# Optimization experiments

Hardware: AMD Instinct MI355X
Metric: run time of the kernel (lower is better)

The kernel has to match this reference:

```python
import jax, jax.numpy as jnp
import numpy as np

B, F, V, D, A, ND = 4096, 26, 100000, 16, 16, 13


def setup_inputs() -> dict:
    key = jax.random.key(0)
    ks = jax.random.split(key, 10)
    dense_input = jax.random.normal(ks[0], (B, ND), dtype=jnp.float32)
    sparse_input = jax.random.randint(ks[1], (B, F), 0, V, dtype=jnp.int32)
    # all fields share feat_num=V, so stack tables into one [F, V, D] array
    embed_tables = jax.random.normal(ks[2], (F, V, D), dtype=jnp.float32) * 0.001
    att_W = jax.random.normal(ks[3], (D, A), dtype=jnp.float32) * (2.0 / (D + A)) ** 0.5
    att_b = jnp.zeros((A,), dtype=jnp.float32)
    att_h = jax.random.normal(ks[4], (A, 1), dtype=jnp.float32) * (2.0 / (A + 1)) ** 0.5
    att_p = jax.random.normal(ks[5], (D, 1), dtype=jnp.float32) * (2.0 / (D + 1)) ** 0.5
    lin_w_dense = jax.random.normal(ks[6], (ND, 1), dtype=jnp.float32) * 0.01
    lin_w_sparse = jax.random.normal(ks[7], (F * D, 1), dtype=jnp.float32) * 0.01
    lin_b = jnp.zeros((1,), dtype=jnp.float32)
    return {"dense_input": dense_input, "sparse_input": sparse_input,
            "embed_tables": embed_tables, "att_W": att_W, "att_b": att_b,
            "att_h": att_h, "att_p": att_p, "lin_w_dense": lin_w_dense,
            "lin_w_sparse": lin_w_sparse, "lin_b": lin_b}


def reference(dense_input, sparse_input, embed_tables, att_W, att_b, att_h,
              att_p, lin_w_dense, lin_w_sparse, lin_b):
    # per-field embedding gather: [B, F, D]
    emb = embed_tables[jnp.arange(F)[None, :], sparse_input]
    sparse_concat = emb.reshape(B, F * D)
    # linear part (Linear(dense, sparse_concat) -> [B, 1])
    linear_result = dense_input @ lin_w_dense + sparse_concat @ lin_w_sparse + lin_b
    # pairwise element-wise products for i < j: [B, P, D], P = F*(F-1)/2
    iu, ju = np.triu_indices(F, k=1)
    ewp = emb[:, iu, :] * emb[:, ju, :]
    # attention MLP over pairs
    att_wx_b = jax.nn.relu(jnp.einsum('bpd,da->bpa', ewp, att_W) + att_b)
    score = jax.nn.softmax(jnp.einsum('bpa,ao->bpo', att_wx_b, att_h), axis=1)  # [B,P,1]
    att_output = jnp.sum(score * ewp, axis=1)  # [B, D]; dropout_rate=0 -> identity
    afm_result = att_output @ att_p  # [B, 1]
    return jax.nn.sigmoid(afm_result + linear_result)
```

## Files before the change

kernel.cpp:

```cpp
#include <hip/hip_runtime.h>
#include <hip/hip_bf16.h>

typedef float v4f    __attribute__((ext_vector_type(4)));
typedef float f32x16 __attribute__((ext_vector_type(16)));
typedef __bf16 bf16x8 __attribute__((ext_vector_type(8)));

#define BATCH 4096
#define NF 26
#define NV 100000
#define ND_ 16
#define NA 16
#define NDENSE 13
#define NPAIR 325
#define ROWP 20
#define WPB 4
#define BLOCK (WPB * 64)
#define NTILE 11

__global__ __launch_bounds__(BLOCK) void afm_kernel(
    const float* __restrict__ dense,
    const int*   __restrict__ sparse,
    const float* __restrict__ tables,
    const float* __restrict__ attW,
    const float* __restrict__ attB,
    const float* __restrict__ attH,
    const float* __restrict__ attP,
    const float* __restrict__ wDense,
    const float* __restrict__ wSparse,
    const float* __restrict__ linB,
    float* __restrict__ out)
{
    __shared__ int sOFF[NPAIR];
    __shared__ __align__(16) float sEmb[WPB][NF * ROWP];
    __shared__ int sIdx[WPB][NF];

    const int tid  = threadIdx.x;
    const int wave = tid >> 6;
    const int lane = tid & 63;
    const int col  = lane & 31;
    const int hi   = lane >> 5;
    const int b    = blockIdx.x * WPB + wave;

    for (int p = tid; p < NPAIR; p += BLOCK) {
        int i = 0, rem = p;
        while (rem >= NF - 1 - i) { rem -= NF - 1 - i; ++i; }
        const int j = i + 1 + rem;
        sOFF[p] = (i * ROWP) | ((j * ROWP) << 16);
    }
    if (lane < NF) sIdx[wave][lane] = sparse[b * NF + lane];
    __syncthreads();

    for (int c = lane; c < (NF * ND_) / 4; c += 64) {
        const int f  = c >> 2;
        const int d4 = (c & 3) << 2;
        const float4 v = *reinterpret_cast<const float4*>(
            tables + ((size_t)f * NV + (size_t)sIdx[wave][f]) * ND_ + d4);
        *reinterpret_cast<float4*>(&sEmb[wave][f * ROWP + d4]) = v;
    }

    bf16x8 afrag;
    #pragma unroll
    for (int t = 0; t < 8; ++t) {
        float a = 0.f;
        if (col < NA)       a = attW[(hi * 8 + t) * NA + col];
        else if (col == NA) a = attP[hi * 8 + t];
        afrag[t] = (__bf16)a;
    }
    float  hreg[8];
    f32x16 cinit = {0.f,0.f,0.f,0.f,0.f,0.f,0.f,0.f,0.f,0.f,0.f,0.f,0.f,0.f,0.f,0.f};
    #pragma unroll
    for (int r = 0; r < 8; ++r) {
        const int k = (r & 3) + 8 * (r >> 2) + 4 * hi;
        hreg[r]  = attH[k];
        cinit[r] = attB[k];
    }

    const float* __restrict__ semb = sEmb[wave];

    float lin = 0.f;
    for (int e = lane; e < NF * ND_; e += 64)
        lin += semb[(e >> 4) * ROWP + (e & 15)] * wSparse[e];
    if (lane < NDENSE)
        lin += dense[b * NDENSE + lane] * wDense[lane];

    float num = 0.f, den = 0.f;
    for (int t = 0; t < NTILE; ++t) {
        const int p     = t * 32 + col;
        const bool valid = (p < NPAIR) && (hi == 0);
        const int pc    = (p < NPAIR) ? p : (NPAIR - 1);
        const int offs  = sOFF[pc];
        const float* ri = semb + (offs & 0xffff) + hi * 8;
        const float* rj = semb + (offs >> 16)    + hi * 8;

        const v4f x0 = *reinterpret_cast<const v4f*>(ri);
        const v4f x1 = *reinterpret_cast<const v4f*>(ri + 4);
        const v4f y0 = *reinterpret_cast<const v4f*>(rj);
        const v4f y1 = *reinterpret_cast<const v4f*>(rj + 4);
        const v4f e0 = x0 * y0;
        const v4f e1 = x1 * y1;

        bf16x8 bfrag;
        bfrag[0] = (__bf16)e0[0]; bfrag[1] = (__bf16)e0[1];
        bfrag[2] = (__bf16)e0[2]; bfrag[3] = (__bf16)e0[3];
        bfrag[4] = (__bf16)e1[0]; bfrag[5] = (__bf16)e1[1];
        bfrag[6] = (__bf16)e1[2]; bfrag[7] = (__bf16)e1[3];

        const f32x16 acc =
            __builtin_amdgcn_mfma_f32_32x32x16_bf16(afrag, bfrag, cinit, 0, 0, 0);

        float sp = 0.f;
        #pragma unroll
        for (int r = 0; r < 8; ++r)
            sp = fmaf(fmaxf(acc[r], 0.f), hreg[r], sp);
        const float sfull = sp + __shfl_xor(sp, 32);

        const float ev = valid ? __expf(sfull) : 0.f;
        num = fmaf(ev, acc[8], num);
        den += ev;
    }

    #pragma unroll
    for (int o = 32; o; o >>= 1) {
        num += __shfl_xor(num, o);
        den += __shfl_xor(den, o);
        lin += __shfl_xor(lin, o);
    }
    if (lane == 0) {
        const float x = num / den + lin + linB[0];
        out[b] = 1.f / (1.f + __expf(-x));
    }
}

extern "C" void kernel_launch(void* const* d_in, const int* in_sizes, int n_in,
                              void* d_out, int out_size, void* d_ws, size_t ws_size,
                              hipStream_t stream) {
    const float* dense   = (const float*)d_in[0];
    const int*   sparse  = (const int*)d_in[1];
    const float* tables  = (const float*)d_in[2];
    const float* attW    = (const float*)d_in[3];
    const float* attB    = (const float*)d_in[4];
    const float* attH    = (const float*)d_in[5];
    const float* attP    = (const float*)d_in[6];
    const float* wDense  = (const float*)d_in[7];
    const float* wSparse = (const float*)d_in[8];
    const float* linB    = (const float*)d_in[9];
    float* out = (float*)d_out;

    const int grid = BATCH / WPB;
    afm_kernel<<<grid, BLOCK, 0, stream>>>(
        dense, sparse, tables, attW, attB, attH, attP,
        wDense, wSparse, linB, out);
}
```

Measured before the change: 15.41 us.

## Drop block barrier and pair table; walk contiguous pairs per lane with cached row

Removes the shared pair-offset table and the block-wide __syncthreads. Sparse indices now stay in registers and reach the gather lanes through a wave shuffle, with only a wave barrier before reading the embeddings. Each lane now handles a contiguous run of pairs, stepping (i, j) incrementally and reloading row i only when it changes, which cuts LDS reads and removes the division-like pair decode from every tile. The trade-off is more divergence when lanes cross row boundaries at different tiles, and reliance on the wave barrier being enough to make the LDS writes visible within the wave.

New measurement: 28.71 us. +86.3%, slower.

```diff
diff --git a/kernel.cpp b/kernel.cpp
--- a/kernel.cpp
+++ b/kernel.cpp
@@ -30,9 +30,7 @@
     const float* __restrict__ linB,
     float* __restrict__ out)
 {
-    __shared__ int sOFF[NPAIR];
     __shared__ __align__(16) float sEmb[WPB][NF * ROWP];
-    __shared__ int sIdx[WPB][NF];
 
     const int tid  = threadIdx.x;
     const int wave = tid >> 6;
@@ -41,21 +39,20 @@
     const int hi   = lane >> 5;
     const int b    = blockIdx.x * WPB + wave;
 
-    for (int p = tid; p < NPAIR; p += BLOCK) {
-        int i = 0, rem = p;
-        while (rem >= NF - 1 - i) { rem -= NF - 1 - i; ++i; }
-        const int j = i + 1 + rem;
-        sOFF[p] = (i * ROWP) | ((j * ROWP) << 16);
-    }
-    if (lane < NF) sIdx[wave][lane] = sparse[b * NF + lane];
-    __syncthreads();
+    int idxreg = 0;
+    if (lane < NF) idxreg = sparse[b * NF + lane];
 
-    for (int c = lane; c < (NF * ND_) / 4; c += 64) {
-        const int f  = c >> 2;
-        const int d4 = (c & 3) << 2;
-        const float4 v = *reinterpret_cast<const float4*>(
-            tables + ((size_t)f * NV + (size_t)sIdx[wave][f]) * ND_ + d4);
-        *reinterpret_cast<float4*>(&sEmb[wave][f * ROWP + d4]) = v;
+    #pragma unroll
+    for (int rnd = 0; rnd < 2; ++rnd) {
+        const int c = lane + rnd * 64;
+        if (c < (NF * ND_) / 4) {
+            const int f  = c >> 2;
+            const int d4 = (c & 3) << 2;
+            const int row = __shfl(idxreg, f);
+            const float4 v = *reinterpret_cast<const float4*>(
+                tables + ((size_t)f * NV + (size_t)row) * ND_ + d4);
+            *reinterpret_cast<float4*>(&sEmb[wave][f * ROWP + d4]) = v;
+        }
     }
 
     bf16x8 afrag;
@@ -75,29 +72,42 @@
         cinit[r] = attB[k];
     }
 
+    __builtin_amdgcn_wave_barrier();
+
     const float* __restrict__ semb = sEmb[wave];
 
     float lin = 0.f;
-    for (int e = lane; e < NF * ND_; e += 64)
-        lin += semb[(e >> 4) * ROWP + (e & 15)] * wSparse[e];
+    #pragma unroll
+    for (int rnd = 0; rnd < 7; ++rnd) {
+        const int e = lane + rnd * 64;
+        if (e < NF * ND_)
+            lin += semb[(e >> 4) * ROWP + (e & 15)] * wSparse[e];
+    }
     if (lane < NDENSE)
         lin += dense[b * NDENSE + lane] * wDense[lane];
 
+    int p0 = col * NTILE;
+    if (p0 > NPAIR - 1) p0 = NPAIR - 1;
+    int i = 0, rem = p0;
+    while (rem >= NF - 1 - i) { rem -= NF - 1 - i; ++i; }
+    int j = i + 1 + rem;
+
     float num = 0.f, den = 0.f;
+    v4f ri0, ri1;
+    bool need_ri = true;
+
     for (int t = 0; t < NTILE; ++t) {
-        const int p     = t * 32 + col;
-        const bool valid = (p < NPAIR) && (hi == 0);
-        const int pc    = (p < NPAIR) ? p : (NPAIR - 1);
-        const int offs  = sOFF[pc];
-        const float* ri = semb + (offs & 0xffff) + hi * 8;
-        const float* rj = semb + (offs >> 16)    + hi * 8;
-
-        const v4f x0 = *reinterpret_cast<const v4f*>(ri);
-        const v4f x1 = *reinterpret_cast<const v4f*>(ri + 4);
+        if (need_ri) {
+            const float* ri = semb + i * ROWP + hi * 8;
+            ri0 = *reinterpret_cast<const v4f*>(ri);
+            ri1 = *reinterpret_cast<const v4f*>(ri + 4);
+            need_ri = false;
+        }
+        const float* rj = semb + j * ROWP + hi * 8;
         const v4f y0 = *reinterpret_cast<const v4f*>(rj);
         const v4f y1 = *reinterpret_cast<const v4f*>(rj + 4);
-        const v4f e0 = x0 * y0;
-        const v4f e1 = x1 * y1;
+        const v4f e0 = ri0 * y0;
+        const v4f e1 = ri1 * y1;
 
         bf16x8 bfrag;
         bfrag[0] = (__bf16)e0[0]; bfrag[1] = (__bf16)e0[1];
@@ -114,9 +124,17 @@
             sp = fmaf(fmaxf(acc[r], 0.f), hreg[r], sp);
         const float sfull = sp + __shfl_xor(sp, 32);
 
+        const bool valid = (col * NTILE + t < NPAIR) && (hi == 0);
         const float ev = valid ? __expf(sfull) : 0.f;
         num = fmaf(ev, acc[8], num);
         den += ev;
+
+        ++j;
+        if (j >= NF) {
+            if (i < NF - 2) { ++i; }
+            j = i + 1;
+            need_ri = true;
+        }
     }
 
     #pragma unroll
```

## Issue embedding gathers before setup and broadcast indices via shuffles

Applied to the files above, without the earlier changes.

Each wave keeps its sparse indices in registers and broadcasts them with wave shuffles instead of staging them in shared memory. That lets the embedding gathers start at kernel entry, before the pair-offset table and weight fragments are built, and the block barrier moves after that setup so gather latency overlaps it. The linear-term loop and the MFMA tile loop are fully unrolled. The ReLU·h reduction is written as packed 2-wide FMAs to encourage packed FP32 instructions. Unrolling raises register pressure and code size.

Result: faster. 14.87 us (-3.5%).

```diff
diff --git a/kernel.cpp b/kernel.cpp
--- a/kernel.cpp
+++ b/kernel.cpp
@@ -1,6 +1,7 @@
 #include <hip/hip_runtime.h>
 #include <hip/hip_bf16.h>
 
+typedef float v2f    __attribute__((ext_vector_type(2)));
 typedef float v4f    __attribute__((ext_vector_type(4)));
 typedef float f32x16 __attribute__((ext_vector_type(16)));
 typedef __bf16 bf16x8 __attribute__((ext_vector_type(8)));
@@ -32,7 +33,6 @@
 {
     __shared__ int sOFF[NPAIR];
     __shared__ __align__(16) float sEmb[WPB][NF * ROWP];
-    __shared__ int sIdx[WPB][NF];
 
     const int tid  = threadIdx.x;
     const int wave = tid >> 6;
@@ -41,21 +41,27 @@
     const int hi   = lane >> 5;
     const int b    = blockIdx.x * WPB + wave;
 
+    int idxreg = 0;
+    if (lane < NF) idxreg = sparse[b * NF + lane];
+
+    #pragma unroll
+    for (int rnd = 0; rnd < 2; ++rnd) {
+        const int c = lane + rnd * 64;
+        if (c < (NF * ND_) / 4) {
+            const int f  = c >> 2;
+            const int d4 = (c & 3) << 2;
+            const int row = __shfl(idxreg, f);
+            const float4 v = *reinterpret_cast<const float4*>(
+                tables + ((size_t)f * NV + (size_t)row) * ND_ + d4);
+            *reinterpret_cast<float4*>(&sEmb[wave][f * ROWP + d4]) = v;
+        }
+    }
+
     for (int p = tid; p < NPAIR; p += BLOCK) {
         int i = 0, rem = p;
         while (rem >= NF - 1 - i) { rem -= NF - 1 - i; ++i; }
         const int j = i + 1 + rem;
         sOFF[p] = (i * ROWP) | ((j * ROWP) << 16);
-    }
-    if (lane < NF) sIdx[wave][lane] = sparse[b * NF + lane];
-    __syncthreads();
-
-    for (int c = lane; c < (NF * ND_) / 4; c += 64) {
-        const int f  = c >> 2;
-        const int d4 = (c & 3) << 2;
-        const float4 v = *reinterpret_cast<const float4*>(
-            tables + ((size_t)f * NV + (size_t)sIdx[wave][f]) * ND_ + d4);
-        *reinterpret_cast<float4*>(&sEmb[wave][f * ROWP + d4]) = v;
     }
 
     bf16x8 afrag;
@@ -75,15 +81,22 @@
         cinit[r] = attB[k];
     }
 
+    __syncthreads();
+
     const float* __restrict__ semb = sEmb[wave];
 
     float lin = 0.f;
-    for (int e = lane; e < NF * ND_; e += 64)
-        lin += semb[(e >> 4) * ROWP + (e & 15)] * wSparse[e];
+    #pragma unroll
+    for (int rnd = 0; rnd < 7; ++rnd) {
+        const int e = lane + rnd * 64;
+        if (e < NF * ND_)
+            lin += semb[(e >> 4) * ROWP + (e & 15)] * wSparse[e];
+    }
     if (lane < NDENSE)
         lin += dense[b * NDENSE + lane] * wDense[lane];
 
     float num = 0.f, den = 0.f;
+    #pragma unroll
     for (int t = 0; t < NTILE; ++t) {
         const int p     = t * 32 + col;
         const bool valid = (p < NPAIR) && (hi == 0);
@@ -108,10 +121,15 @@
         const f32x16 acc =
             __builtin_amdgcn_mfma_f32_32x32x16_bf16(afrag, bfrag, cinit, 0, 0, 0);
 
-        float sp = 0.f;
+        v2f sp2 = {0.f, 0.f};
         #pragma unroll
-        for (int r = 0; r < 8; ++r)
-            sp = fmaf(fmaxf(acc[r], 0.f), hreg[r], sp);
+        for (int r = 0; r < 4; ++r) {
+            v2f z;  z.x = acc[2 * r];  z.y = acc[2 * r + 1];
+            v2f zr; zr.x = fmaxf(z.x, 0.f); zr.y = fmaxf(z.y, 0.f);
+            v2f h;  h.x = hreg[2 * r]; h.y = hreg[2 * r + 1];
+            sp2 = zr * h + sp2;
+        }
+        const float sp = sp2.x + sp2.y;
         const float sfull = sp + __shfl_xor(sp, 32);
 
         const float ev = valid ? __expf(sfull) : 0.f;
```
